# Optimization experiments

Measured on AMD Instinct MI355X. Metric: run time of the kernel, lower is better.

## Reference

```python
import jax, jax.numpy as jnp
import numpy as np

SEQ = 2048
D_MODEL = 1024
N_HEADS = 16
TOP_K = 64
Q_LR = 128
KV_LR = 128
ROPE_DIM = 32
V_DIM = 64
IDX_DIM = 64
# Mamba2 indexer block: expand=1, headdim=32, d_state=64, d_conv=4
D_INNER = D_MODEL
M_HD = 32
M_NH = D_INNER // M_HD  # 32 ssm heads
M_DS = 64
M_DC = 4
CONV_CH = D_INNER + 2 * M_DS  # 1152
IN_DIM = 2 * D_INNER + 2 * M_DS + M_NH  # 2208


def _silu(x):
    return x * jax.nn.sigmoid(x)


def _mamba2(x, in_w, conv_w, conv_b, dt_bias, A_log, D, norm_w, out_w):
    # Minimal Mamba2 (SSD) recurrent forward: in_proj -> causal depthwise conv
    # on (x, B, C) -> selective scan with scalar-per-head A -> gated RMSNorm -> out_proj.
    L = x.shape[0]
    zxbcdt = x @ in_w.T  # [L, IN_DIM]
    z = zxbcdt[:, :D_INNER]
    xBC = zxbcdt[:, D_INNER:D_INNER + CONV_CH]
    dt = zxbcdt[:, -M_NH:]
    # causal depthwise conv1d, kernel M_DC
    xp = jnp.pad(xBC, ((M_DC - 1, 0), (0, 0)))
    conv = conv_b
    for k in range(M_DC):
        conv = conv + xp[k:k + L] * conv_w[:, k]
    xBC = _silu(conv)
    xs = xBC[:, :D_INNER].reshape(L, M_NH, M_HD)          # [L,h,p]
    B = xBC[:, D_INNER:D_INNER + M_DS]                     # [L,n]
    C = xBC[:, D_INNER + M_DS:]                            # [L,n]
    dt = jax.nn.softplus(dt + dt_bias)                     # [L,h]
    dA = jnp.exp(dt * (-jnp.exp(A_log)))                   # [L,h]
    dBx = jnp.einsum('lh,lhp,ln->lhpn', dt, xs, B)         # [L,h,p,n]

    def step(h, inp):
        dA_t, dBx_t, C_t = inp
        h = h * dA_t[:, None, None] + dBx_t
        y_t = jnp.einsum('hpn,n->hp', h, C_t)
        return h, y_t

    h0 = jnp.zeros((M_NH, M_HD, M_DS), x.dtype)
    _, y = jax.lax.scan(step, h0, (dA, dBx, C))            # y: [L,h,p]
    y = y + D[:, None] * xs
    y = y.reshape(L, D_INNER) * _silu(z)                   # gated
    y = y * jax.lax.rsqrt(jnp.mean(y * y, axis=-1, keepdims=True) + 1e-5) * norm_w
    return y @ out_w.T


def _make_rope(L):
    inv = 1.0 / (10000.0 ** (jnp.arange(0, ROPE_DIM, 2, dtype=jnp.float32) / ROPE_DIM))
    ang = jnp.arange(L, dtype=jnp.float32)[:, None] * inv  # [L, ROPE/2]
    return jnp.sin(ang), jnp.cos(ang)


def _apply_rope(x, sin, cos):
    # x: [L, H, ROPE_DIM]; rotate-half convention
    x1, x2 = jnp.split(x, 2, axis=-1)
    s = sin[:, None, :]
    c = cos[:, None, :]
    return jnp.concatenate([x1 * c - x2 * s, x1 * s + x2 * c], axis=-1)


def _forward(x, idx_in_w, idx_conv_w, idx_conv_b, idx_dt_bias, idx_A_log, idx_D,
             idx_norm_w, idx_out_w, idx_q_w, idx_k_w, q_down_w, q_up_w, q_rope_w,
             kv_down_w, kv_up_w, k_rope_w, out_w):
    L = x.shape[0]
    # --- Mamba2 indexer scores ---
    x_mamba = _mamba2(x, idx_in_w, idx_conv_w, idx_conv_b, idx_dt_bias,
                      idx_A_log, idx_D, idx_norm_w, idx_out_w)
    q_idx = x_mamba @ idx_q_w.T                            # [L, IDX_DIM]
    k_idx = x @ idx_k_w.T                                  # [L, IDX_DIM]
    scores = (q_idx @ k_idx.T) * (IDX_DIM ** -0.5)         # [L, L]
    mask = jnp.tril(jnp.ones((L, L), dtype=bool))
    scores = jnp.where(mask, scores, -jnp.inf)
    k_val = min(TOP_K, L)
    _, indices = jax.lax.top_k(scores, k_val)              # [L, K]
    # --- MLA low-rank projections ---
    c_q = x @ q_down_w.T                                   # [L, Q_LR]
    q_content = (c_q @ q_up_w.T).reshape(L, N_HEADS, V_DIM)
    q_rope = (c_q @ q_rope_w.T).reshape(L, N_HEADS, ROPE_DIM)
    c_kv = x @ kv_down_w.T                                 # [L, KV_LR]
    kv = c_kv @ kv_up_w.T                                  # [L, 2*H*V]
    k_content_flat, v_flat = jnp.split(kv, 2, axis=-1)
    k_content = k_content_flat.reshape(L, N_HEADS, V_DIM)
    v = v_flat.reshape(L, N_HEADS, V_DIM)
    k_rope_shared = (x @ k_rope_w.T)[:, None, :]           # [L, 1, ROPE]
    sin, cos = _make_rope(L)
    q_rope_rot = _apply_rope(q_rope, sin, cos)
    k_rope_rot = jnp.tile(_apply_rope(k_rope_shared, sin, cos), (1, N_HEADS, 1))
    q_final = jnp.concatenate([q_content, q_rope_rot], axis=-1)  # [L,H,dk]
    k_final = jnp.concatenate([k_content, k_rope_rot], axis=-1)  # [L,H,dk]
    # --- top-k gather sparse attention ---
    k_sparse = k_final[indices]                            # [L,K,H,dk]
    v_sparse = v[indices]                                  # [L,K,H,dv]
    dk = k_final.shape[-1]
    logits = jnp.einsum('lhd,lkhd->lhk', q_final, k_sparse) * (dk ** -0.5)
    w = jax.nn.softmax(logits, axis=-1)
    attn = jnp.einsum('lhk,lkhd->lhd', w, v_sparse).reshape(L, N_HEADS * V_DIM)
    return attn @ out_w.T


def setup_inputs() -> dict:
    key = jax.random.key(0)
    ks = jax.random.split(key, 16)

    def g(k, shape, s=0.02):
        return jax.random.normal(k, shape, jnp.float32) * s

    return {
        "x": jax.random.normal(ks[0], (SEQ, D_MODEL), jnp.float32),
        "idx_in_w": g(ks[1], (IN_DIM, D_MODEL)),
        "idx_conv_w": g(ks[2], (CONV_CH, M_DC), 0.2),
        "idx_conv_b": jnp.zeros((CONV_CH,), jnp.float32),
        "idx_dt_bias": g(ks[3], (M_NH,), 0.1),
        "idx_A_log": jnp.log(jnp.arange(1, M_NH + 1, dtype=jnp.float32)),
        "idx_D": jnp.ones((M_NH,), jnp.float32),
        "idx_norm_w": jnp.ones((D_INNER,), jnp.float32),
        "idx_out_w": g(ks[4], (D_MODEL, D_INNER)),
        "idx_q_w": g(ks[5], (IDX_DIM, D_MODEL)),
        "idx_k_w": g(ks[6], (IDX_DIM, D_MODEL)),
        "q_down_w": g(ks[7], (Q_LR, D_MODEL)),
        "q_up_w": g(ks[8], (N_HEADS * V_DIM, Q_LR)),
        "q_rope_w": g(ks[9], (N_HEADS * ROPE_DIM, Q_LR)),
        "kv_down_w": g(ks[10], (KV_LR, D_MODEL)),
        "kv_up_w": g(ks[11], (2 * N_HEADS * V_DIM, KV_LR)),
        "k_rope_w": g(ks[12], (ROPE_DIM, D_MODEL)),
        "out_w": g(ks[13], (D_MODEL, N_HEADS * V_DIM)),
    }


def reference(x, idx_in_w, idx_conv_w, idx_conv_b, idx_dt_bias, idx_A_log, idx_D,
              idx_norm_w, idx_out_w, idx_q_w, idx_k_w, q_down_w, q_up_w, q_rope_w,
              kv_down_w, kv_up_w, k_rope_w, out_w):
    return _forward(x, idx_in_w, idx_conv_w, idx_conv_b, idx_dt_bias, idx_A_log,
                    idx_D, idx_norm_w, idx_out_w, idx_q_w, idx_k_w, q_down_w,
                    q_up_w, q_rope_w, kv_down_w, kv_up_w, k_rope_w, out_w)
```

## Files before the change

kernel.cpp:

```cpp
#include <hip/hip_runtime.h>
#include <math.h>

constexpr int L      = 2048;
constexpr int NH     = 16;
constexpr int DINNER = 1024;
constexpr int MNH    = 32;
constexpr int CONVCH = 1152;
constexpr int INDIMP = 2304;
constexpr int CHUNK  = 64;
constexpr int NCH    = 32;

using bf16x8 = __attribute__((ext_vector_type(8))) short;
using f32x4  = __attribute__((ext_vector_type(4))) float;

__device__ __forceinline__ f32x4 splat4(float x) { return (f32x4){x, x, x, x}; }

__device__ __forceinline__ unsigned short f2bf(float f) {
  unsigned u = __float_as_uint(f);
  return (unsigned short)((u + 0x7fffu + ((u >> 16) & 1u)) >> 16);
}
__device__ __forceinline__ float bf2f(unsigned short h) {
  return __uint_as_float((unsigned)h << 16);
}

__global__ __launch_bounds__(256) void gemm_f32_v3(
    const float* __restrict__ A, const float* __restrict__ W,
    float* __restrict__ C, int M, int N, int K, int tri) {
  __shared__ float As[16][132];
  __shared__ float Ws[16][132];
  int tid = threadIdx.x;
  int bm = blockIdx.y * 128, bn = blockIdx.x * 128;
  if (tri && bn > bm + 127) return;
  int kper = K / gridDim.z;
  int kb = blockIdx.z * kper, ke = kb + kper;
  int lr = tid >> 1;
  int lh = (tid & 1) * 8;
  int tx = tid & 15, ty = tid >> 4;
  bool wok = (bn + lr < N);
  const float* arow = A + (size_t)(bm + lr) * K + lh;
  const float* wrow = W + (size_t)(bn + lr) * K + lh;
  float4 a0, a1, w0, w1;
  auto gload = [&](int k0) {
    a0 = *(const float4*)(arow + k0);
    a1 = *(const float4*)(arow + k0 + 4);
    w0 = make_float4(0.f, 0.f, 0.f, 0.f); w1 = w0;
    if (wok) {
      w0 = *(const float4*)(wrow + k0);
      w1 = *(const float4*)(wrow + k0 + 4);
    }
  };
  f32x4 acc0[8] = {}, acc1[8] = {};
  gload(kb);
  for (int k0 = kb; k0 < ke; k0 += 16) {
    __syncthreads();
    As[lh+0][lr]=a0.x; As[lh+1][lr]=a0.y; As[lh+2][lr]=a0.z; As[lh+3][lr]=a0.w;
    As[lh+4][lr]=a1.x; As[lh+5][lr]=a1.y; As[lh+6][lr]=a1.z; As[lh+7][lr]=a1.w;
    Ws[lh+0][lr]=w0.x; Ws[lh+1][lr]=w0.y; Ws[lh+2][lr]=w0.z; Ws[lh+3][lr]=w0.w;
    Ws[lh+4][lr]=w1.x; Ws[lh+5][lr]=w1.y; Ws[lh+6][lr]=w1.z; Ws[lh+7][lr]=w1.w;
    __syncthreads();
    if (k0 + 16 < ke) gload(k0 + 16);
#pragma unroll
    for (int kk = 0; kk < 16; ++kk) {
      f32x4 b0 = *(const f32x4*)&Ws[kk][tx * 4];
      f32x4 b1 = *(const f32x4*)&Ws[kk][64 + tx * 4];
      f32x4 al = *(const f32x4*)&As[kk][ty * 8];
      f32x4 ah = *(const f32x4*)&As[kk][ty * 8 + 4];
#pragma unroll
      for (int i = 0; i < 4; ++i) {
        acc0[i]     += splat4(al[i]) * b0;
        acc1[i]     += splat4(al[i]) * b1;
        acc0[i + 4] += splat4(ah[i]) * b0;
        acc1[i + 4] += splat4(ah[i]) * b1;
      }
    }
  }
  bool single = (gridDim.z == 1);
#pragma unroll
  for (int i = 0; i < 8; ++i) {
    int row = bm + ty * 8 + i;
    float* crow = C + (size_t)row * N;
    int c0 = bn + tx * 4, c1 = bn + 64 + tx * 4;
    if (c0 + 3 < N) {
      if (single) *(f32x4*)(crow + c0) = acc0[i];
      else {
        atomicAdd(crow + c0 + 0, acc0[i][0]); atomicAdd(crow + c0 + 1, acc0[i][1]);
        atomicAdd(crow + c0 + 2, acc0[i][2]); atomicAdd(crow + c0 + 3, acc0[i][3]);
      }
    }
    if (c1 + 3 < N) {
      if (single) *(f32x4*)(crow + c1) = acc1[i];
      else {
        atomicAdd(crow + c1 + 0, acc1[i][0]); atomicAdd(crow + c1 + 1, acc1[i][1]);
        atomicAdd(crow + c1 + 2, acc1[i][2]); atomicAdd(crow + c1 + 3, acc1[i][3]);
      }
    }
  }
}

__global__ __launch_bounds__(256) void gemm_f32_dual(
    const float* __restrict__ A0, const float* __restrict__ W0, float* __restrict__ C0,
    const float* __restrict__ A1, const float* __restrict__ W1, float* __restrict__ C1,
    int M, int N, int K, int S) {
  __shared__ float As[16][132];
  __shared__ float Ws[16][132];
  int tid = threadIdx.x;
  int bm = blockIdx.y * 128, bn = blockIdx.x * 128;
  int pair = (int)blockIdx.z >= S;
  int zi = blockIdx.z - pair * S;
  const float* A = pair ? A1 : A0;
  const float* W = pair ? W1 : W0;
  float* C = pair ? C1 : C0;
  int kper = K / S;
  int kb = zi * kper, ke = kb + kper;
  int lr = tid >> 1;
  int lh = (tid & 1) * 8;
  int tx = tid & 15, ty = tid >> 4;
  bool wok = (bn + lr < N);
  const float* arow = A + (size_t)(bm + lr) * K + lh;
  const float* wrow = W + (size_t)(bn + lr) * K + lh;
  float4 a0, a1, w0, w1;
  auto gload = [&](int k0) {
    a0 = *(const float4*)(arow + k0);
    a1 = *(const float4*)(arow + k0 + 4);
    w0 = make_float4(0.f, 0.f, 0.f, 0.f); w1 = w0;
    if (wok) {
      w0 = *(const float4*)(wrow + k0);
      w1 = *(const float4*)(wrow + k0 + 4);
    }
  };
  f32x4 acc0[8] = {}, acc1[8] = {};
  gload(kb);
  for (int k0 = kb; k0 < ke; k0 += 16) {
    __syncthreads();
    As[lh+0][lr]=a0.x; As[lh+1][lr]=a0.y; As[lh+2][lr]=a0.z; As[lh+3][lr]=a0.w;
    As[lh+4][lr]=a1.x; As[lh+5][lr]=a1.y; As[lh+6][lr]=a1.z; As[lh+7][lr]=a1.w;
    Ws[lh+0][lr]=w0.x; Ws[lh+1][lr]=w0.y; Ws[lh+2][lr]=w0.z; Ws[lh+3][lr]=w0.w;
    Ws[lh+4][lr]=w1.x; Ws[lh+5][lr]=w1.y; Ws[lh+6][lr]=w1.z; Ws[lh+7][lr]=w1.w;
    __syncthreads();
    if (k0 + 16 < ke) gload(k0 + 16);
#pragma unroll
    for (int kk = 0; kk < 16; ++kk) {
      f32x4 b0 = *(const f32x4*)&Ws[kk][tx * 4];
      f32x4 b1 = *(const f32x4*)&Ws[kk][64 + tx * 4];
      f32x4 al = *(const f32x4*)&As[kk][ty * 8];
      f32x4 ah = *(const f32x4*)&As[kk][ty * 8 + 4];
#pragma unroll
      for (int i = 0; i < 4; ++i) {
        acc0[i]     += splat4(al[i]) * b0;
        acc1[i]     += splat4(al[i]) * b1;
        acc0[i + 4] += splat4(ah[i]) * b0;
        acc1[i + 4] += splat4(ah[i]) * b1;
      }
    }
  }
#pragma unroll
  for (int i = 0; i < 8; ++i) {
    int row = bm + ty * 8 + i;
    float* crow = C + (size_t)row * N;
    int c0 = bn + tx * 4, c1 = bn + 64 + tx * 4;
    if (c0 + 3 < N) {
      atomicAdd(crow + c0 + 0, acc0[i][0]); atomicAdd(crow + c0 + 1, acc0[i][1]);
      atomicAdd(crow + c0 + 2, acc0[i][2]); atomicAdd(crow + c0 + 3, acc0[i][3]);
    }
    if (c1 + 3 < N) {
      atomicAdd(crow + c1 + 0, acc1[i][0]); atomicAdd(crow + c1 + 1, acc1[i][1]);
      atomicAdd(crow + c1 + 2, acc1[i][2]); atomicAdd(crow + c1 + 3, acc1[i][3]);
    }
  }
}

__global__ __launch_bounds__(256) void gemm_bf16_kernel(
    const unsigned short* __restrict__ A, const unsigned short* __restrict__ W,
    float* __restrict__ C, int M, int N, int K, int lda, int ldb, int ldc) {
  __shared__ unsigned short As[2][128 * 64];
  __shared__ unsigned short Ws[2][128 * 64];
  int tid = threadIdx.x;
  int bx = blockIdx.x, by = blockIdx.y;
  int nxy = gridDim.x * gridDim.y;
  if ((nxy & 7) == 0) {
    int lin = by * gridDim.x + bx;
    int cpx = nxy >> 3;
    int swz = (lin & 7) * cpx + (lin >> 3);
    bx = swz % gridDim.x;
    by = swz / gridDim.x;
  }
  int bm = by * 128, bn = bx * 128;
  int kper = K / gridDim.z;
  int k_begin = blockIdx.z * kper;
  int k_end = k_begin + kper;
  int wv = tid >> 6, lane = tid & 63;
  int wrow = (wv >> 1) * 64, wcol = (wv & 1) * 64;
  int lrow = lane & 15, quad = lane >> 4;

  f32x4 acc[4][4] = {};

  auto stage = [&](int b, int k0) {
#pragma unroll
    for (int it = 0; it < 4; ++it) {
      int s = it * 256 + tid;
      int r = s >> 3;
      int q = (s & 7) ^ (r & 7);
      const unsigned short* ga = A + (size_t)(bm + r) * lda + k0 + q * 8;
      const unsigned short* gw = W + (size_t)(bn + r) * ldb + k0 + q * 8;
      __builtin_amdgcn_global_load_lds((const __attribute__((address_space(1))) void*)ga,
                                       (__attribute__((address_space(3))) void*)&As[b][s * 8], 16, 0, 0);
      __builtin_amdgcn_global_load_lds((const __attribute__((address_space(1))) void*)gw,
                                       (__attribute__((address_space(3))) void*)&Ws[b][s * 8], 16, 0, 0);
    }
  };

  stage(0, k_begin);
  int cur = 0;
  for (int k0 = k_begin; k0 < k_end; k0 += 64) {
    __syncthreads();
    if (k0 + 64 < k_end) stage(cur ^ 1, k0 + 64);
#pragma unroll
    for (int ks = 0; ks < 2; ++ks) {
      bf16x8 af[4], wf[4];
#pragma unroll
      for (int i = 0; i < 4; ++i) {
        int ra = wrow + i * 16 + lrow;
        int qa = (ks * 4 + quad) ^ (ra & 7);
        af[i] = *(const bf16x8*)&As[cur][(ra * 8 + qa) * 8];
        int rw = wcol + i * 16 + lrow;
        int qw = (ks * 4 + quad) ^ (rw & 7);
        wf[i] = *(const bf16x8*)&Ws[cur][(rw * 8 + qw) * 8];
      }
#pragma unroll
      for (int i = 0; i < 4; ++i)
#pragma unroll
        for (int j = 0; j < 4; ++j)
          acc[i][j] = __builtin_amdgcn_mfma_f32_16x16x32_bf16(af[i], wf[j], acc[i][j], 0, 0, 0);
    }
    cur ^= 1;
  }
  bool single = (gridDim.z == 1);
#pragma unroll
  for (int i = 0; i < 4; ++i)
#pragma unroll
    for (int j = 0; j < 4; ++j)
#pragma unroll
      for (int r = 0; r < 4; ++r) {
        int row = bm + wrow + i * 16 + quad * 4 + r;
        int col = bn + wcol + j * 16 + lrow;
        float v = acc[i][j][r];
        if (single) C[(size_t)row * ldc + col] = v;
        else atomicAdd(&C[(size_t)row * ldc + col], v);
      }
}

__global__ __launch_bounds__(256) void gemm_bf16_dual(
    const unsigned short* __restrict__ A0, const unsigned short* __restrict__ W0,
    float* __restrict__ C0,
    const unsigned short* __restrict__ A1, const unsigned short* __restrict__ W1,
    float* __restrict__ C1,
    int nx0, int ldc0, int ldc1, int K, int ld) {
  __shared__ unsigned short As[2][128 * 64];
  __shared__ unsigned short Ws[2][128 * 64];
  int tid = threadIdx.x;
  int bx = blockIdx.x, by = blockIdx.y;
  int pair = bx >= nx0;
  int bxl = pair ? bx - nx0 : bx;
  const unsigned short* A = pair ? A1 : A0;
  const unsigned short* W = pair ? W1 : W0;
  float* C = pair ? C1 : C0;
  int ldc = pair ? ldc1 : ldc0;
  int bm = by * 128, bn = bxl * 128;
  int wv = tid >> 6, lane = tid & 63;
  int wrow = (wv >> 1) * 64, wcol = (wv & 1) * 64;
  int lrow = lane & 15, quad = lane >> 4;

  f32x4 acc[4][4] = {};

  auto stage = [&](int b, int k0) {
#pragma unroll
    for (int it = 0; it < 4; ++it) {
      int s = it * 256 + tid;
      int r = s >> 3;
      int q = (s & 7) ^ (r & 7);
      const unsigned short* ga = A + (size_t)(bm + r) * ld + k0 + q * 8;
      const unsigned short* gw = W + (size_t)(bn + r) * ld + k0 + q * 8;
      __builtin_amdgcn_global_load_lds((const __attribute__((address_space(1))) void*)ga,
                                       (__attribute__((address_space(3))) void*)&As[b][s * 8], 16, 0, 0);
      __builtin_amdgcn_global_load_lds((const __attribute__((address_space(1))) void*)gw,
                                       (__attribute__((address_space(3))) void*)&Ws[b][s * 8], 16, 0, 0);
    }
  };

  stage(0, 0);
  int cur = 0;
  for (int k0 = 0; k0 < K; k0 += 64) {
    __syncthreads();
    if (k0 + 64 < K) stage(cur ^ 1, k0 + 64);
#pragma unroll
    for (int ks = 0; ks < 2; ++ks) {
      bf16x8 af[4], wf[4];
#pragma unroll
      for (int i = 0; i < 4; ++i) {
        int ra = wrow + i * 16 + lrow;
        int qa = (ks * 4 + quad) ^ (ra & 7);
        af[i] = *(const bf16x8*)&As[cur][(ra * 8 + qa) * 8];
        int rw = wcol + i * 16 + lrow;
        int qw = (ks * 4 + quad) ^ (rw & 7);
        wf[i] = *(const bf16x8*)&Ws[cur][(rw * 8 + qw) * 8];
      }
#pragma unroll
      for (int i = 0; i < 4; ++i)
#pragma unroll
        for (int j = 0; j < 4; ++j)
          acc[i][j] = __builtin_amdgcn_mfma_f32_16x16x32_bf16(af[i], wf[j], acc[i][j], 0, 0, 0);
    }
    cur ^= 1;
  }
#pragma unroll
  for (int i = 0; i < 4; ++i)
#pragma unroll
    for (int j = 0; j < 4; ++j)
#pragma unroll
      for (int r = 0; r < 4; ++r) {
        int row = bm + wrow + i * 16 + quad * 4 + r;
        int col = bn + wcol + j * 16 + lrow;
        C[(size_t)row * ldc + col] = acc[i][j][r];
      }
}

__global__ __launch_bounds__(256) void prep_weights_kernel(
    const float* __restrict__ x, unsigned short* __restrict__ x_trip,
    const float* __restrict__ idx_in_w, unsigned short* __restrict__ w_in_trip,
    const float* __restrict__ q_down_w, const float* __restrict__ kv_down_w,
    const float* __restrict__ k_rope_w, unsigned short* __restrict__ w3down,
    const float* __restrict__ q_up_w, const float* __restrict__ q_rope_w,
    unsigned short* __restrict__ wqups,
    const float* __restrict__ kv_up_w, unsigned short* __restrict__ wkvup,
    const float* __restrict__ idx_out_w, float* __restrict__ out_w_T) {
  __shared__ float tsh[32][33];
  int bid = blockIdx.x;
  if (bid >= 20736) {
    int b = bid - 20736;
    int bx = b & 31, by = b >> 5;
    int tx = threadIdx.x & 31, ty8 = threadIdx.x >> 5;
    for (int r = ty8; r < 32; r += 8)
      tsh[r][tx] = idx_out_w[(size_t)(by * 32 + r) * 1024 + bx * 32 + tx];
    __syncthreads();
    for (int r = ty8; r < 32; r += 8)
      out_w_T[(size_t)(bx * 32 + r) * 1024 + by * 32 + tx] = tsh[tx][r];
    return;
  }
  int i = bid * 256 + threadIdx.x;
  if (i < 2097152) {
    float f = x[i];
    unsigned short h = f2bf(f);
    float r1 = f - bf2f(h);
    unsigned short m = f2bf(r1);
    unsigned short l = f2bf(r1 - bf2f(m));
    size_t o = (size_t)i * 6;
    x_trip[o] = h; x_trip[o + 1] = m; x_trip[o + 2] = l;
    x_trip[o + 3] = h; x_trip[o + 4] = m; x_trip[o + 5] = h;
  } else if (i < 4456448) {
    int j = i - 2097152;
    int n = j >> 10, k = j & 1023;
    unsigned short h = 0, m = 0, l = 0;
    if (n < 2208) {
      float f = idx_in_w[(size_t)n * 1024 + k];
      h = f2bf(f);
      float r1 = f - bf2f(h);
      m = f2bf(r1);
      l = f2bf(r1 - bf2f(m));
    }
    size_t o = (size_t)j * 6;
    w_in_trip[o] = h; w_in_trip[o + 1] = h; w_in_trip[o + 2] = h;
    w_in_trip[o + 3] = m; w_in_trip[o + 4] = m; w_in_trip[o + 5] = l;
  } else {
    int j2 = i - 4456448;
    const float* src; unsigned short* dst; int rows, K; size_t obase; int idx;
    if (j2 < 393216) {
      int r = j2 >> 17;
      idx = j2 & 131071;
      K = 1024;
      src = (r == 0) ? q_down_w : (r == 1) ? kv_down_w : k_rope_w;
      rows = (r == 2) ? 32 : 128;
      dst = w3down; obase = (size_t)(r * 131072 + idx) * 3;
    } else if (j2 < 524288) {
      idx = j2 - 393216; K = 128; src = q_up_w; rows = 1024;
      dst = wqups; obase = (size_t)idx * 3;
    } else if (j2 < 589824) {
      idx = j2 - 524288; K = 128; src = q_rope_w; rows = 512;
      dst = wqups; obase = (size_t)393216 + (size_t)idx * 3;
    } else {
      idx = j2 - 589824; K = 128; src = kv_up_w; rows = 2048;
      dst = wkvup; obase = (size_t)idx * 3;
    }
    int n = idx / K, k = idx - n * K;
    unsigned short hi = 0, lo = 0;
    if (n < rows) {
      float f = src[(size_t)n * K + k];
      hi = f2bf(f);
      lo = f2bf(f - bf2f(hi));
    }
    dst[obase] = hi; dst[obase + 1] = hi; dst[obase + 2] = lo;
  }
}

__global__ __launch_bounds__(256) void post_inproj_kernel(
    const float* __restrict__ out_w, unsigned short* __restrict__ w_outp,
    const float* __restrict__ zxbcdt, const float* __restrict__ conv_w,
    const float* __restrict__ conv_b, float* __restrict__ xBC,
    const float* __restrict__ dt_bias, const float* __restrict__ A_log,
    float* __restrict__ dt, float* __restrict__ logdA) {
  int i = blockIdx.x * 256 + threadIdx.x;
  if (i < 1048576) {
    float f = out_w[i];
    unsigned short hi = f2bf(f);
    unsigned short lo = f2bf(f - bf2f(hi));
    size_t o = (size_t)i * 3;
    w_outp[o] = hi; w_outp[o + 1] = hi; w_outp[o + 2] = lo;
  } else if (i < 3407872) {
    int idx = i - 1048576;
    int l = idx / CONVCH, c = idx - l * CONVCH;
    float acc = conv_b[c];
#pragma unroll
    for (int k = 0; k < 4; ++k) {
      int ls = l - 3 + k;
      if (ls >= 0) acc += zxbcdt[(size_t)ls * INDIMP + DINNER + c] * conv_w[c * 4 + k];
    }
    xBC[idx] = acc / (1.f + expf(-acc));
  } else {
    int idx = i - 3407872;
    int l = idx >> 5, h = idx & 31;
    float xv = zxbcdt[(size_t)l * INDIMP + 2176 + h] + dt_bias[h];
    float sp = fmaxf(xv, 0.f) + log1pf(expf(-fabsf(xv)));
    dt[idx] = sp;
    logdA[idx] = sp * -expf(A_log[h]);
  }
}

__global__ __launch_bounds__(256) void conv_augA_kernel(
    const float* __restrict__ src, unsigned short* __restrict__ dst,
    int total, int K, int sld) {
  int i = blockIdx.x * 256 + threadIdx.x;
  if (i >= total) return;
  int m = i / K, k = i - m * K;
  float f = src[(size_t)m * sld + k];
  unsigned short hi = f2bf(f);
  unsigned short lo = f2bf(f - bf2f(hi));
  size_t o = ((size_t)m * K + k) * 3;
  dst[o] = hi; dst[o + 1] = lo; dst[o + 2] = hi;
}
__global__ __launch_bounds__(256) void conv_augA2_kernel(
    const float* __restrict__ c3, unsigned short* __restrict__ dq,
    unsigned short* __restrict__ dkv) {
  int i = blockIdx.x * 256 + threadIdx.x;
  if (i >= 2048 * 256) return;
  int m = i >> 8, k = i & 255;
  float f = c3[(size_t)m * 384 + k];
  unsigned short hi = f2bf(f);
  unsigned short lo = f2bf(f - bf2f(hi));
  if (k < 128) {
    size_t o = ((size_t)m * 128 + k) * 3;
    dq[o] = hi; dq[o + 1] = lo; dq[o + 2] = hi;
  } else {
    size_t o = ((size_t)m * 128 + (k - 128)) * 3;
    dkv[o] = hi; dkv[o + 1] = lo; dkv[o + 2] = hi;
  }
}

__global__ __launch_bounds__(256) void chunk_G_kernel(
    const float* __restrict__ xBC, float* __restrict__ G,
    const float* __restrict__ logdA, float* __restrict__ lcd) {
  int c = blockIdx.x, tid = threadIdx.x;
  if (c >= NCH) {
    int i = (c - NCH) * 256 + tid;
    int cc = i >> 5, h = i & 31;
    float s = 0.f;
    for (int t = 0; t < CHUNK; ++t) {
      s += logdA[(cc * CHUNK + t) * MNH + h];
      lcd[(size_t)i * CHUNK + t] = s;
    }
    return;
  }
  __shared__ float BsT[64][68];
  __shared__ float Cs[64][65];
  int t = tid >> 2, q = tid & 3;
  const float* row = xBC + (size_t)(c * 64 + t) * CONVCH + DINNER;
#pragma unroll
  for (int j = 0; j < 16; j += 4) {
    float4 b = *(const float4*)(row + q * 16 + j);
    BsT[q * 16 + j + 0][t] = b.x; BsT[q * 16 + j + 1][t] = b.y;
    BsT[q * 16 + j + 2][t] = b.z; BsT[q * 16 + j + 3][t] = b.w;
    float4 cv = *(const float4*)(row + 64 + q * 16 + j);
    Cs[t][q * 16 + j + 0] = cv.x; Cs[t][q * 16 + j + 1] = cv.y;
    Cs[t][q * 16 + j + 2] = cv.z; Cs[t][q * 16 + j + 3] = cv.w;
  }
  __syncthreads();
  int s0 = q * 16;
  f32x4 g0 = {}, g1 = {}, g2 = {}, g3 = {};
  for (int n = 0; n < 64; ++n) {
    f32x4 cv = splat4(Cs[t][n]);
    g0 += cv * *(const f32x4*)&BsT[n][s0];
    g1 += cv * *(const f32x4*)&BsT[n][s0 + 4];
    g2 += cv * *(const f32x4*)&BsT[n][s0 + 8];
    g3 += cv * *(const f32x4*)&BsT[n][s0 + 12];
  }
  float* gp = G + ((size_t)c * 64 + t) * 64 + s0;
  *(f32x4*)gp = g0; *(f32x4*)(gp + 4) = g1; *(f32x4*)(gp + 8) = g2; *(f32x4*)(gp + 12) = g3;
}

__global__ __launch_bounds__(256) void scan_local_kernel(
    const float* __restrict__ xBC, const float* __restrict__ dt,
    const float* __restrict__ lcd, float* __restrict__ hstate) {
  int c = blockIdx.x >> 5, h = blockIdx.x & 31;
  int tid = threadIdx.x;
  __shared__ float Bs[64][68];
  __shared__ float xss[64][36];
  __shared__ float w2s[64];
  int t0 = c * CHUNK;
  int t = tid >> 2, q = tid & 3;
  const float* row = xBC + (size_t)(t0 + t) * CONVCH;
#pragma unroll
  for (int j = 0; j < 16; j += 4)
    *(float4*)&Bs[t][q * 16 + j] = *(const float4*)(row + DINNER + q * 16 + j);
  if (q < 2) {
#pragma unroll
    for (int j = 0; j < 16; j += 4)
      *(float4*)&xss[t][q * 16 + j] = *(const float4*)(row + h * 32 + q * 16 + j);
  }
  if (tid < 64) {
    const float* lc = lcd + ((size_t)c * 32 + h) * CHUNK;
    w2s[tid] = expf(lc[63] - lc[tid]) * dt[(t0 + tid) * MNH + h];
  }
  __syncthreads();
  int n = tid >> 2, pg = (tid & 3) * 8;
  f32x4 h0 = {}, h1 = {};
  for (int s = 0; s < 64; ++s) {
    f32x4 wb = splat4(w2s[s] * Bs[s][n]);
    h0 += wb * *(const f32x4*)&xss[s][pg];
    h1 += wb * *(const f32x4*)&xss[s][pg + 4];
  }
  float* hp = hstate + ((size_t)c * 32 + h) * 2048 + n * 32 + pg;
  *(f32x4*)hp = h0; *(f32x4*)(hp + 4) = h1;
}

__global__ __launch_bounds__(256) void scan_combine_kernel(
    float* __restrict__ hstate, const float* __restrict__ lcd) {
  int i = blockIdx.x * 256 + threadIdx.x;
  int h = i >> 11;
  float H = 0.f;
  for (int c = 0; c < NCH; ++c) {
    float hl = hstate[(size_t)c * 65536 + i];
    hstate[(size_t)c * 65536 + i] = H;
    float P = expf(lcd[((size_t)c * 32 + h) * CHUNK + CHUNK - 1]);
    H = H * P + hl;
  }
}

__global__ __launch_bounds__(256) void scan_y_kernel(
    const float* __restrict__ xBC, const float* __restrict__ G,
    const float* __restrict__ dt, const float* __restrict__ lcd,
    const float* __restrict__ hstate, float* __restrict__ y) {
  int c = blockIdx.x >> 5, h = blockIdx.x & 31;
  int tid = threadIdx.x;
  __shared__ float Ms[64][65];
  __shared__ float Cs[64][65];
  __shared__ float xss[64][36];
  __shared__ float Hss[64][36];
  __shared__ float lcds[64], dts[64];
  int t0 = c * CHUNK;
  int t = tid >> 2, q = tid & 3;
  const float* row = xBC + (size_t)(t0 + t) * CONVCH;
#pragma unroll
  for (int j = 0; j < 16; j += 4) {
    float4 cv = *(const float4*)(row + DINNER + 64 + q * 16 + j);
    Cs[t][q * 16 + j + 0] = cv.x; Cs[t][q * 16 + j + 1] = cv.y;
    Cs[t][q * 16 + j + 2] = cv.z; Cs[t][q * 16 + j + 3] = cv.w;
  }
  if (q < 2) {
#pragma unroll
    for (int j = 0; j < 16; j += 4)
      *(float4*)&xss[t][q * 16 + j] = *(const float4*)(row + h * 32 + q * 16 + j);
  }
  {
    const float* gp = G + ((size_t)c * 64 + t) * 64 + q * 16;
#pragma unroll
    for (int j = 0; j < 16; j += 4) {
      float4 g = *(const float4*)(gp + j);
      Ms[t][q * 16 + j + 0] = g.x; Ms[t][q * 16 + j + 1] = g.y;
      Ms[t][q * 16 + j + 2] = g.z; Ms[t][q * 16 + j + 3] = g.w;
    }
  }
  {
    const float* hp = hstate + ((size_t)c * 32 + h) * 2048 + tid * 8;
    int n = tid >> 2, p0 = (tid & 3) * 8;
    *(float4*)&Hss[n][p0]     = *(const float4*)hp;
    *(float4*)&Hss[n][p0 + 4] = *(const float4*)(hp + 4);
  }
  if (tid < 64) {
    lcds[tid] = lcd[((size_t)c * 32 + h) * CHUNK + tid];
    dts[tid]  = dt[(t0 + tid) * MNH + h];
  }
  __syncthreads();
  {
    int s0 = q * 16;
#pragma unroll
    for (int j = 0; j < 16; ++j) {
      int s = s0 + j;
      float m = (s <= t) ? expf(lcds[t] - lcds[s]) * dts[s] * Ms[t][s] : 0.f;
      Ms[t][s] = m;
    }
  }
  __syncthreads();
  int pg = q * 8;
  f32x4 y0 = {}, y1 = {}, a0 = {}, a1 = {};
  for (int s = 0; s < 64; ++s) {
    f32x4 m = splat4(Ms[t][s]);
    y0 += m * *(const f32x4*)&xss[s][pg];
    y1 += m * *(const f32x4*)&xss[s][pg + 4];
  }
  for (int n = 0; n < 64; ++n) {
    f32x4 cn = splat4(Cs[t][n]);
    a0 += cn * *(const f32x4*)&Hss[n][pg];
    a1 += cn * *(const f32x4*)&Hss[n][pg + 4];
  }
  f32x4 cd = splat4(expf(lcds[t]));
  y0 += cd * a0; y1 += cd * a1;
  float* yp = y + (size_t)(t0 + t) * DINNER + h * 32 + pg;
  *(f32x4*)yp = y0; *(f32x4*)(yp + 4) = y1;
}

__global__ __launch_bounds__(256) void gatenorm_kernel(
    const float* __restrict__ y_ssm, const float* __restrict__ xBC,
    const float* __restrict__ zxbcdt, const float* __restrict__ Dv,
    const float* __restrict__ norm_w, float* __restrict__ out) {
  int l = blockIdx.x, tid = threadIdx.x;
  float vals[4];
  float ss = 0.f;
#pragma unroll
  for (int i = 0; i < 4; ++i) {
    int d = tid + i * 256;
    int h = d >> 5;
    float v = y_ssm[(size_t)l * DINNER + d] + Dv[h] * xBC[(size_t)l * CONVCH + d];
    float z = zxbcdt[(size_t)l * INDIMP + d];
    v *= z / (1.f + expf(-z));
    vals[i] = v;
    ss += v * v;
  }
#pragma unroll
  for (int off = 32; off > 0; off >>= 1) ss += __shfl_xor(ss, off);
  __shared__ float sred[4];
  if ((tid & 63) == 0) sred[tid >> 6] = ss;
  __syncthreads();
  float tot = sred[0] + sred[1] + sred[2] + sred[3];
  float scale = rsqrtf(tot * (1.f / 1024.f) + 1e-5f);
#pragma unroll
  for (int i = 0; i < 4; ++i) {
    int d = tid + i * 256;
    out[(size_t)l * DINNER + d] = vals[i] * scale * norm_w[d];
  }
}

__global__ __launch_bounds__(256) void topk_kernel(
    const float* __restrict__ scores, int* __restrict__ out_idx) {
  int l = blockIdx.x, tid = threadIdx.x;
  if (l < 64) {
    if (tid < 64) out_idx[l * 64 + tid] = tid;
    return;
  }
  int n = l + 1;
  const float* row = scores + (size_t)l * L;
  __shared__ int hist[256];
  __shared__ unsigned sel_prefix;
  __shared__ int sel_remaining;
  __shared__ int cnt_g, cnt_e;
  __shared__ int eq_list[128];
  if (tid == 0) { cnt_g = 0; cnt_e = 0; }
  unsigned prefix = 0;
  int remaining = 64;
  for (int pass = 0; pass < 4; ++pass) {
    int shift = 24 - 8 * pass;
    unsigned himask = (pass == 0) ? 0u : (0xFFFFFFFFu << (shift + 8));
    hist[tid] = 0;
    __syncthreads();
    for (int j = tid; j < n; j += 256) {
      unsigned u = __float_as_uint(row[j]);
      unsigned key = (u & 0x80000000u) ? ~u : (u | 0x80000000u);
      if (((key ^ prefix) & himask) == 0)
        atomicAdd(&hist[(key >> shift) & 255], 1);
    }
    __syncthreads();
    if (tid == 0) {
      int cum = 0, b = 255;
      for (; b >= 0; --b) {
        cum += hist[b];
        if (cum >= remaining) break;
      }
      sel_prefix = prefix | ((unsigned)b << shift);
      sel_remaining = remaining - (cum - hist[b]);
    }
    __syncthreads();
    prefix = sel_prefix;
    remaining = sel_remaining;
    __syncthreads();
  }
  unsigned T = prefix;
  for (int j = tid; j < n; j += 256) {
    unsigned u = __float_as_uint(row[j]);
    unsigned key = (u & 0x80000000u) ? ~u : (u | 0x80000000u);
    if (key > T) {
      int p = atomicAdd(&cnt_g, 1);
      out_idx[l * 64 + p] = j;
    } else if (key == T) {
      int p = atomicAdd(&cnt_e, 1);
      if (p < 128) eq_list[p] = j;
    }
  }
  __syncthreads();
  if (tid == 0) {
    int G = cnt_g;
    int E = remaining;
    int m = cnt_e < 128 ? cnt_e : 128;
    for (int e = 0; e < E; ++e) {
      int best = 0, bj = 0x7fffffff;
      for (int i = 0; i < m; ++i)
        if (eq_list[i] < bj) { bj = eq_list[i]; best = i; }
      out_idx[l * 64 + G + e] = bj;
      eq_list[best] = 0x7fffffff;
    }
  }
}

__global__ __launch_bounds__(128) void rope_pack_kernel(
    const float* __restrict__ qbuf, const float* __restrict__ kv,
    const float* __restrict__ c3,
    float* __restrict__ q_final, float* __restrict__ k_final) {
  int l = blockIdx.x, tid = threadIdx.x;
  __shared__ float s_s[16], s_c[16];
  if (tid < 16) {
    float inv = powf(10000.f, -(float)tid / 16.f);
    float ang = (float)l * inv;
    s_s[tid] = sinf(ang);
    s_c[tid] = cosf(ang);
  }
  __syncthreads();
  const float* qrow = qbuf + (size_t)l * 1536;
  const float* krow = c3 + (size_t)l * 384 + 256;
  for (int e = tid; e < NH * 96; e += 128) {
    int hh = e / 96, d = e - hh * 96;
    float qv, kvv;
    if (d < 64) {
      qv  = qrow[hh * 64 + d];
      kvv = kv[(size_t)l * 2048 + hh * 64 + d];
    } else {
      int r = d - 64;
      if (r < 16) {
        float q1 = qrow[1024 + hh * 32 + r];
        float q2 = qrow[1024 + hh * 32 + 16 + r];
        qv = q1 * s_c[r] - q2 * s_s[r];
        float k1 = krow[r];
        float k2 = krow[16 + r];
        kvv = k1 * s_c[r] - k2 * s_s[r];
      } else {
        int rr = r - 16;
        float q1 = qrow[1024 + hh * 32 + rr];
        float q2 = qrow[1024 + hh * 32 + 16 + rr];
        qv = q1 * s_s[rr] + q2 * s_c[rr];
        float k1 = krow[rr];
        float k2 = krow[16 + rr];
        kvv = k1 * s_s[rr] + k2 * s_c[rr];
      }
    }
    q_final[(size_t)l * 1536 + e] = qv;
    k_final[(size_t)l * 1536 + e] = kvv;
  }
}

__global__ __launch_bounds__(256) void attn_kernel(
    const float* __restrict__ q_final, const float* __restrict__ k_final,
    const float* __restrict__ kv, const int* __restrict__ idx,
    unsigned short* __restrict__ attn_aug) {
  int b = blockIdx.x;
  int l = (b & 7) * 256 + (b >> 3);
  int tid = threadIdx.x;
  int h = tid >> 4;
  int s = tid & 15;
  __shared__ __align__(16) float lg[16][64];
  __shared__ int iks[64];

  if (tid < 64) iks[tid] = idx[l * 64 + tid];

  const float* qrow = q_final + (size_t)l * 1536 + h * 96 + s * 2;
  float q0 = qrow[0],  q1 = qrow[1];
  float q2 = qrow[32], q3 = qrow[33];
  float q4 = qrow[64], q5 = qrow[65];
  __syncthreads();

#pragma unroll 4
  for (int k = 0; k < 64; ++k) {
    const float* kr = k_final + (size_t)iks[k] * 1536 + h * 96 + s * 2;
    float2 a = *(const float2*)kr;
    float2 b2 = *(const float2*)(kr + 32);
    float2 c = *(const float2*)(kr + 64);
    float d = q0 * a.x + q1 * a.y + q2 * b2.x + q3 * b2.y + q4 * c.x + q5 * c.y;
    d += __shfl_xor(d, 1);
    d += __shfl_xor(d, 2);
    d += __shfl_xor(d, 4);
    d += __shfl_xor(d, 8);
    if (s == 0) lg[h][k] = d * 0.10206207261596575f;
  }
  __syncthreads();

  f32x4 lv = *(const f32x4*)&lg[h][s * 4];
  float m = fmaxf(fmaxf(lv[0], lv[1]), fmaxf(lv[2], lv[3]));
#pragma unroll
  for (int off = 1; off < 16; off <<= 1) m = fmaxf(m, __shfl_xor(m, off));
  f32x4 ev;
  ev[0] = expf(lv[0] - m); ev[1] = expf(lv[1] - m);
  ev[2] = expf(lv[2] - m); ev[3] = expf(lv[3] - m);
  float ssum = ev[0] + ev[1] + ev[2] + ev[3];
#pragma unroll
  for (int off = 1; off < 16; off <<= 1) ssum += __shfl_xor(ssum, off);
  float inv = 1.f / ssum;
  lg[h][s * 4 + 0] = ev[0] * inv;
  lg[h][s * 4 + 1] = ev[1] * inv;
  lg[h][s * 4 + 2] = ev[2] * inv;
  lg[h][s * 4 + 3] = ev[3] * inv;
  __syncthreads();

  f32x4 acc = {};
#pragma unroll 4
  for (int k = 0; k < 64; ++k) {
    const float* vr = kv + (size_t)iks[k] * 2048 + 1024 + tid * 4;
    f32x4 v = *(const f32x4*)vr;
    acc += splat4(lg[h][k]) * v;
  }

#pragma unroll
  for (int i = 0; i < 4; ++i) {
    float a = acc[i];
    unsigned short hi = f2bf(a);
    unsigned short lo = f2bf(a - bf2f(hi));
    size_t o = ((size_t)l * 1024 + tid * 4 + i) * 3;
    attn_aug[o] = hi; attn_aug[o + 1] = lo; attn_aug[o + 2] = hi;
  }
}

extern "C" void kernel_launch(void* const* d_in, const int* in_sizes, int n_in,
                              void* d_out, int out_size, void* d_ws, size_t ws_size,
                              hipStream_t stream) {
  const float* x          = (const float*)d_in[0];
  const float* idx_in_w   = (const float*)d_in[1];
  const float* idx_conv_w = (const float*)d_in[2];
  const float* idx_conv_b = (const float*)d_in[3];
  const float* idx_dt_b   = (const float*)d_in[4];
  const float* idx_A_log  = (const float*)d_in[5];
  const float* idx_D      = (const float*)d_in[6];
  const float* idx_norm_w = (const float*)d_in[7];
  const float* idx_out_w  = (const float*)d_in[8];
  const float* idx_q_w    = (const float*)d_in[9];
  const float* idx_k_w    = (const float*)d_in[10];
  const float* q_down_w   = (const float*)d_in[11];
  const float* q_up_w     = (const float*)d_in[12];
  const float* q_rope_w   = (const float*)d_in[13];
  const float* kv_down_w  = (const float*)d_in[14];
  const float* kv_up_w    = (const float*)d_in[15];
  const float* k_rope_w   = (const float*)d_in[16];
  const float* out_w      = (const float*)d_in[17];
  float* out = (float*)d_out;

  float* p = (float*)d_ws;
  float* segA = p; p += 4718592;
  float* segB = p; p += 2359296;
  float* dtb = p; p += 65536;
  float* logdA = p; p += 65536;
  float* lcdb = p; p += 65536;
  int*   idxb = (int*)p; p += 131072;
  float* segD = p; p += 4194304;
  float* segBig1 = p; p += 6291456;
  float* segBig2 = p; p += 7077888;
  float* segH = p; p += 3145728;
  unsigned short* w_3down_aug = (unsigned short*)p; p += 589824;
  unsigned short* w_qups_aug  = (unsigned short*)p; p += 294912;
  unsigned short* w_kvup_aug  = (unsigned short*)p; p += 393216;
  unsigned short* c_q_aug     = (unsigned short*)p; p += 393216;
  unsigned short* c_kv_aug    = (unsigned short*)p; p += 393216;
  float* Gbuf = p; p += 131072;

  float* zxbcdt = segA;
  float* scores = segA;
  float* qbuf   = segA;
  float* xBC    = segB;
  float* q_idx  = segB;
  float* k_idx  = segB + 131072;
  float* c3     = segB + 262144;
  float* y_ssm  = segD;
  float* hstate = segD + 2097152;
  float* kvb    = segD;
  unsigned short* x_trip     = (unsigned short*)segBig1;
  unsigned short* w_outp_aug = (unsigned short*)segBig1;
  unsigned short* w_in_trip  = (unsigned short*)segBig2;
  float* y_norm  = segBig2;
  unsigned short* x_aug = (unsigned short*)segBig2;
  float* q_final = segBig2;
  unsigned short* attn_aug = (unsigned short*)(segBig2 + 3145728);
  float* out_w_T = segH;
  float* qwpad   = segH + 1048576;
  float* Wq      = segH + 1179648;
  float* k_final = segH;

  dim3 blk(256);
  auto cdiv = [](int a, int b) { return (a + b - 1) / b; };
  auto gemmf3 = [&](const float* A, const float* W, float* C, int M, int N, int K, int S, int tri) {
    dim3 grid(cdiv(N, 128), M / 128, S);
    hipLaunchKernelGGL(gemm_f32_v3, grid, blk, 0, stream, A, W, C, M, N, K, tri);
  };
  auto gemmb = [&](const unsigned short* A, const unsigned short* W, float* C,
                   int M, int N, int K, int lda, int ldb, int ldc, int S) {
    dim3 grid(N / 128, M / 128, S);
    hipLaunchKernelGGL(gemm_bf16_kernel, grid, blk, 0, stream, A, W, C, M, N, K, lda, ldb, ldc);
  };

  hipLaunchKernelGGL(prep_weights_kernel, dim3(21760), blk, 0, stream,
                     x, x_trip, idx_in_w, w_in_trip,
                     q_down_w, kv_down_w, k_rope_w, w_3down_aug,
                     q_up_w, q_rope_w, w_qups_aug, kv_up_w, w_kvup_aug,
                     idx_out_w, out_w_T);
  hipMemsetAsync(qwpad, 0, 262144 * 4, stream);
  hipMemcpyAsync(qwpad, idx_q_w, (size_t)64 * 1024 * 4, hipMemcpyDeviceToDevice, stream);
  gemmf3(qwpad, out_w_T, Wq, 128, 1024, 1024, 8, 0);

  hipMemsetAsync(zxbcdt, 0, (size_t)L * INDIMP * 4, stream);
  gemmb(x_trip, w_in_trip, zxbcdt, 2048, 2304, 6144, 6144, 6144, INDIMP, 2);
  hipLaunchKernelGGL(post_inproj_kernel, dim3(13568), blk, 0, stream,
                     out_w, w_outp_aug, zxbcdt, idx_conv_w, idx_conv_b, xBC,
                     idx_dt_b, idx_A_log, dtb, logdA);
  hipLaunchKernelGGL(chunk_G_kernel, dim3(NCH + 4), blk, 0, stream,
                     xBC, Gbuf, logdA, lcdb);
  hipLaunchKernelGGL(scan_local_kernel, dim3(NCH * MNH), blk, 0, stream,
                     xBC, dtb, lcdb, hstate);
  hipLaunchKernelGGL(scan_combine_kernel, dim3(256), blk, 0, stream, hstate, lcdb);
  hipLaunchKernelGGL(scan_y_kernel, dim3(NCH * MNH), blk, 0, stream,
                     xBC, Gbuf, dtb, lcdb, hstate, y_ssm);
  hipLaunchKernelGGL(gatenorm_kernel, dim3(L), blk, 0, stream,
                     y_ssm, xBC, zxbcdt, idx_D, idx_norm_w, y_norm);

  hipMemsetAsync(q_idx, 0, 262144 * 4, stream);
  {
    dim3 grid(1, 16, 32);
    hipLaunchKernelGGL(gemm_f32_dual, grid, blk, 0, stream,
                       y_norm, Wq, q_idx, x, idx_k_w, k_idx, 2048, 64, 1024, 16);
  }
  gemmf3(q_idx, k_idx, scores, 2048, 2048, 64, 1, 1);
  hipLaunchKernelGGL(topk_kernel, dim3(L), blk, 0, stream, scores, idxb);

  hipLaunchKernelGGL(conv_augA_kernel, dim3(cdiv(2048 * 1024, 256)), blk, 0, stream,
                     x, x_aug, 2048 * 1024, 1024, 1024);
  hipMemsetAsync(c3, 0, 786432 * 4, stream);
  gemmb(x_aug, w_3down_aug, c3, 2048, 384, 3072, 3072, 3072, 384, 8);
  hipLaunchKernelGGL(conv_augA2_kernel, dim3(cdiv(2048 * 256, 256)), blk, 0, stream,
                     c3, c_q_aug, c_kv_aug);
  {
    dim3 grid(28, 16, 1);
    hipLaunchKernelGGL(gemm_bf16_dual, grid, blk, 0, stream,
                       c_q_aug, w_qups_aug, qbuf,
                       c_kv_aug, w_kvup_aug, kvb,
                       12, 1536, 2048, 384, 384);
  }
  hipLaunchKernelGGL(rope_pack_kernel, dim3(L), dim3(128), 0, stream,
                     qbuf, kvb, c3, q_final, k_final);

  hipLaunchKernelGGL(attn_kernel, dim3(L), blk, 0, stream,
                     q_final, k_final, kvb, idxb, attn_aug);
  hipMemsetAsync(out, 0, (size_t)out_size * 4, stream);
  gemmb(attn_aug, w_outp_aug, out, 2048, 1024, 3072, 3072, 3072, 1024, 4);
}
```

Baseline: 645.8 us.

## Use 256x256-tile bf16 GEMM with 4-stage direct-to-LDS pipeline for in_proj

```diff
diff --git a/kernel.cpp b/kernel.cpp
--- a/kernel.cpp
+++ b/kernel.cpp
@@ -249,6 +249,102 @@
       }
 }
 
+__global__ __launch_bounds__(512) void gemm_bf16_256_kernel(
+    const unsigned short* __restrict__ A, const unsigned short* __restrict__ W,
+    float* __restrict__ C, int K, int lda, int ldc) {
+  __shared__ unsigned short As[4][256 * 32];
+  __shared__ unsigned short Ws[4][256 * 32];
+  int tid = threadIdx.x;
+  int bx = blockIdx.x, by = blockIdx.y;
+  int nxy = gridDim.x * gridDim.y;
+  if ((nxy & 7) == 0) {
+    int lin = by * gridDim.x + bx;
+    int cpx = nxy >> 3;
+    int swz = (lin & 7) * cpx + (lin >> 3);
+    bx = swz % gridDim.x;
+    by = swz / gridDim.x;
+  }
+  int bm = by * 256, bn = bx * 256;
+  int kper = K / gridDim.z;
+  int kb = blockIdx.z * kper;
+  int U = kper >> 5;
+  int wave = tid >> 6, lane = tid & 63;
+  int wr = wave >> 2, wc = wave & 3;
+  int lrow = lane & 15, quad = lane >> 4;
+
+  f32x4 acc[8][4] = {};
+
+  auto stage = [&](int cell, int u) {
+    int k0 = kb + (u << 5);
+#pragma unroll
+    for (int rd = 0; rd < 2; ++rd) {
+      int s = rd * 512 + tid;
+      int r = s >> 2;
+      int q = (s & 3) ^ (r & 3);
+      const unsigned short* ga = A + (size_t)(bm + r) * lda + k0 + q * 8;
+      __builtin_amdgcn_global_load_lds((const __attribute__((address_space(1))) void*)ga,
+          (__attribute__((address_space(3))) void*)&As[cell][s * 8], 16, 0, 0);
+    }
+#pragma unroll
+    for (int rd = 0; rd < 2; ++rd) {
+      int s = rd * 512 + tid;
+      int r = s >> 2;
+      int q = (s & 3) ^ (r & 3);
+      const unsigned short* gw = W + (size_t)(bn + r) * lda + k0 + q * 8;
+      __builtin_amdgcn_global_load_lds((const __attribute__((address_space(1))) void*)gw,
+          (__attribute__((address_space(3))) void*)&Ws[cell][s * 8], 16, 0, 0);
+    }
+  };
+
+  auto compute = [&](int cell) {
+    bf16x8 af[8], wf[4];
+#pragma unroll
+    for (int m = 0; m < 8; ++m) {
+      int ra = wr * 128 + m * 16 + lrow;
+      af[m] = *(const bf16x8*)&As[cell][((ra << 2) + (quad ^ (ra & 3))) * 8];
+    }
+#pragma unroll
+    for (int n = 0; n < 4; ++n) {
+      int rw = wc * 64 + n * 16 + lrow;
+      wf[n] = *(const bf16x8*)&Ws[cell][((rw << 2) + (quad ^ (rw & 3))) * 8];
+    }
+#pragma unroll
+    for (int m = 0; m < 8; ++m)
+#pragma unroll
+      for (int n = 0; n < 4; ++n)
+        acc[m][n] = __builtin_amdgcn_mfma_f32_16x16x32_bf16(af[m], wf[n], acc[m][n], 0, 0, 0);
+  };
+
+  stage(0, 0); stage(1, 1); stage(2, 2);
+  for (int u = 0; u + 3 < U; ++u) {
+    __builtin_amdgcn_s_barrier();
+    asm volatile("" ::: "memory");
+    stage((u + 3) & 3, u + 3);
+    asm volatile("s_waitcnt vmcnt(12)" ::: "memory");
+    __builtin_amdgcn_s_barrier();
+    asm volatile("" ::: "memory");
+    compute(u & 3);
+  }
+  for (int u = U - 3; u < U; ++u) {
+    __builtin_amdgcn_s_barrier();
+    asm volatile("s_waitcnt vmcnt(0)" ::: "memory");
+    __builtin_amdgcn_s_barrier();
+    asm volatile("" ::: "memory");
+    compute(u & 3);
+  }
+
+#pragma unroll
+  for (int m = 0; m < 8; ++m)
+#pragma unroll
+    for (int n = 0; n < 4; ++n)
+#pragma unroll
+      for (int rr = 0; rr < 4; ++rr) {
+        int row = bm + wr * 128 + m * 16 + quad * 4 + rr;
+        int col = bn + wc * 64 + n * 16 + lrow;
+        atomicAdd(&C[(size_t)row * ldc + col], acc[m][n][rr]);
+      }
+}
+
 __global__ __launch_bounds__(256) void gemm_bf16_dual(
     const unsigned short* __restrict__ A0, const unsigned short* __restrict__ W0,
     float* __restrict__ C0,
@@ -927,7 +1023,11 @@
   gemmf3(qwpad, out_w_T, Wq, 128, 1024, 1024, 8, 0);
 
   hipMemsetAsync(zxbcdt, 0, (size_t)L * INDIMP * 4, stream);
-  gemmb(x_trip, w_in_trip, zxbcdt, 2048, 2304, 6144, 6144, 6144, INDIMP, 2);
+  {
+    dim3 grid(9, 8, 3);
+    hipLaunchKernelGGL(gemm_bf16_256_kernel, grid, dim3(512), 0, stream,
+                       x_trip, w_in_trip, zxbcdt, 6144, 6144, INDIMP);
+  }
   hipLaunchKernelGGL(post_inproj_kernel, dim3(13568), blk, 0, stream,
                      out_w, w_outp_aug, zxbcdt, idx_conv_w, idx_conv_b, xBC,
                      idx_dt_b, idx_A_log, dtb, logdA);
```

Result: no change. 639.1 us (-1.0%).
